# Performance work log

Measured on AMD Instinct MI355X. Metric: run time of the kernel, lower is better.

Reference implementation:

```python
import jax, jax.numpy as jnp
import numpy as np

B, T, IN, H, OUT = 64, 256, 512, 1024, 512

def setup_inputs() -> dict:
    key = jax.random.key(0)
    k1, k2, k3, k4 = jax.random.split(key, 4)
    xs = jax.random.normal(k1, (B, T, IN), dtype=jnp.float32)
    # fused gate projections (order: i, f, g, o), scaled like lecun_normal-ish init
    Wi = jax.random.normal(k2, (IN, 4 * H), dtype=jnp.float32) * (1.0 / np.sqrt(IN))
    Wh = jax.random.normal(k3, (H, 4 * H), dtype=jnp.float32) * (1.0 / np.sqrt(H))
    b = jnp.zeros((4 * H,), dtype=jnp.float32)
    Wo = jax.random.normal(k4, (H, OUT), dtype=jnp.float32) * (1.0 / np.sqrt(H))
    bo = jnp.zeros((OUT,), dtype=jnp.float32)
    return {"xs": xs, "Wi": Wi, "Wh": Wh, "b": b, "Wo": Wo, "bo": bo}

def _lstm_scan(xs, Wi, Wh, b):
    # Precompute the input projection for all timesteps at once: [B, T, 4H]
    xp = jnp.einsum('bti,ih->bth', xs, Wi)
    xp = jnp.transpose(xp, (1, 0, 2))  # [T, B, 4H] for scan over time
    h0 = jnp.zeros((xs.shape[0], Wh.shape[0]), dtype=xs.dtype)
    c0 = jnp.zeros_like(h0)
    Hdim = Wh.shape[0]

    def step(carry, xp_t):
        c, h = carry
        gates = xp_t + h @ Wh + b  # [B, 4H]
        i, f, g, o = jnp.split(gates, 4, axis=-1)  # flax order: i, f, g, o
        c_new = jax.nn.sigmoid(f) * c + jax.nn.sigmoid(i) * jnp.tanh(g)
        h_new = jax.nn.sigmoid(o) * jnp.tanh(c_new)
        return (c_new, h_new), h_new

    (_, _), hs = jax.lax.scan(step, (c0, h0), xp)
    return jnp.transpose(hs, (1, 0, 2))  # [B, T, H]

def reference(xs, Wi, Wh, b, Wo, bo):
    zs = _lstm_scan(xs, Wi, Wh, b)          # [B, T, H]
    logits = jnp.einsum('bth,ho->bto', zs, Wo) + bo  # [B, T, OUT]
    return logits
```

## Files before the change

### kernel.cpp

```cpp
#include <hip/hip_runtime.h>
#include <hip/hip_cooperative_groups.h>


#define B_   64
#define T_   256
#define IN_  512
#define H_   1024
#define G4_  4096
#define OUT_ 512
#define KTOT 1536

typedef __bf16 bf8v  __attribute__((ext_vector_type(8)));
typedef float  f4v   __attribute__((ext_vector_type(4)));

__device__ __forceinline__ float sigm(float x) { return 1.f / (1.f + __expf(-x)); }
__device__ __forceinline__ float tanh_f(float x) { return 1.f - 2.f / (__expf(2.f * x) + 1.f); }

__device__ __forceinline__ void store_bf16_wt(__bf16* p, __bf16 v) {
    union { __bf16 b; unsigned short s; } cv; cv.b = v;
    unsigned w = cv.s;
    asm volatile("global_store_short %0, %1, off sc0 sc1"
                 :: "v"(p), "v"(w) : "memory");
}

__device__ __forceinline__ void grid_barrier(unsigned* flags, int t, int blk) {
    __syncthreads();
    const unsigned tgt = (unsigned)(t + 1);
    if (threadIdx.x < 64) {
        if (threadIdx.x == 0) {
            unsigned* p = &flags[blk * 16];
            asm volatile("global_store_dword %0, %1, off sc0 sc1"
                         :: "v"(p), "v"(tgt) : "memory");
        }
        const int lane = threadIdx.x;
        for (;;) {
            unsigned m0 = __hip_atomic_load(&flags[(lane * 4 + 0) * 16],
                                            __ATOMIC_RELAXED, __HIP_MEMORY_SCOPE_AGENT);
            unsigned m1 = __hip_atomic_load(&flags[(lane * 4 + 1) * 16],
                                            __ATOMIC_RELAXED, __HIP_MEMORY_SCOPE_AGENT);
            unsigned m2 = __hip_atomic_load(&flags[(lane * 4 + 2) * 16],
                                            __ATOMIC_RELAXED, __HIP_MEMORY_SCOPE_AGENT);
            unsigned m3 = __hip_atomic_load(&flags[(lane * 4 + 3) * 16],
                                            __ATOMIC_RELAXED, __HIP_MEMORY_SCOPE_AGENT);
            bool ok = (m0 >= tgt) & (m1 >= tgt) & (m2 >= tgt) & (m3 >= tgt);
            if (__all(ok)) break;
            __builtin_amdgcn_s_sleep(1);
        }
        __builtin_amdgcn_fence(__ATOMIC_ACQUIRE, "agent");
    }
    __syncthreads();
}

__global__ void __launch_bounds__(256)
lstm_fused(const float* __restrict__ xs, const float* __restrict__ Wi,
           const float* __restrict__ Wh, const float* __restrict__ bias,
           const float* __restrict__ Wo, const float* __restrict__ bo,
           float* __restrict__ out, __bf16* __restrict__ hws,
           unsigned* __restrict__ flags)
{
    __shared__ __bf16 Wlds[16][KTOT + 8];
    __shared__ float  gbuf[64][17];
    __shared__ float  obuf[4][16][17];

    const int tid = threadIdx.x;
    const int blk = blockIdx.x;
    const int j0  = blk * 4;
    const int ob0 = (blk >> 5) * 8;
    const int oc0 = (blk & 31) * 16;

    for (int idx = tid; idx < 16 * KTOT; idx += 256) {
        int k = idx >> 4, c = idx & 15;
        int gc = (c >> 2) * H_ + j0 + (c & 3);
        float w = (k < IN_) ? Wi[(size_t)k * G4_ + gc]
                            : Wh[(size_t)(k - IN_) * G4_ + gc];
        Wlds[c][k] = (__bf16)w;
    }
    __syncthreads();

    const int lane = tid & 63;
    const int wave = tid >> 6;
    const int c    = lane & 15;
    const int quad = lane >> 4;
    const int rowA = wave * 16 + c;
    const int kq   = quad * 8;

    const float biasv = bias[(c >> 2) * H_ + j0 + (c & 3)];

    bf8v wof[8];
    #pragma unroll
    for (int kk = 0; kk < 8; ++kk) {
        int kbase = wave * 256 + kk * 32 + kq;
        #pragma unroll
        for (int j = 0; j < 8; ++j)
            wof[kk][j] = (__bf16)Wo[(size_t)(kbase + j) * OUT_ + oc0 + c];
    }

    float c_reg = 0.f;
    const int bb = tid >> 2;
    const int jo = tid & 3;

    for (int t = 0; t < T_; ++t) {
        const __bf16* hhi_p = hws + (size_t)(t & 1) * (2 * B_ * H_);
        const __bf16* hlo_p = hhi_p + B_ * H_;
        __bf16* hhi_c = hws + (size_t)((t + 1) & 1) * (2 * B_ * H_);
        __bf16* hlo_c = hhi_c + B_ * H_;

        f4v acc0 = {0.f, 0.f, 0.f, 0.f};
        f4v acc1 = {0.f, 0.f, 0.f, 0.f};
        const float* xrow = xs + ((size_t)rowA * T_ + t) * IN_ + kq;
        #pragma unroll
        for (int ks = 0; ks < 16; ++ks) {
            f4v v0 = *(const f4v*)(xrow + ks * 32);
            f4v v1 = *(const f4v*)(xrow + ks * 32 + 4);
            bf8v ah, al;
            #pragma unroll
            for (int j = 0; j < 4; ++j) {
                __bf16 h0 = (__bf16)v0[j], h1 = (__bf16)v1[j];
                ah[j] = h0;  ah[4 + j] = h1;
                al[j]     = (__bf16)(v0[j] - (float)h0);
                al[4 + j] = (__bf16)(v1[j] - (float)h1);
            }
            bf8v w = *(const bf8v*)&Wlds[c][ks * 32 + kq];
            acc0 = __builtin_amdgcn_mfma_f32_16x16x32_bf16(ah, w, acc0, 0, 0, 0);
            acc1 = __builtin_amdgcn_mfma_f32_16x16x32_bf16(al, w, acc1, 0, 0, 0);
        }
        if (t > 0) {
            const __bf16* hh = hhi_p + (size_t)rowA * H_ + kq;
            const __bf16* hl = hlo_p + (size_t)rowA * H_ + kq;
            #pragma unroll
            for (int ks = 0; ks < 32; ++ks) {
                bf8v ah = *(const bf8v*)(hh + ks * 32);
                bf8v al = *(const bf8v*)(hl + ks * 32);
                bf8v w  = *(const bf8v*)&Wlds[c][IN_ + ks * 32 + kq];
                acc0 = __builtin_amdgcn_mfma_f32_16x16x32_bf16(ah, w, acc0, 0, 0, 0);
                acc1 = __builtin_amdgcn_mfma_f32_16x16x32_bf16(al, w, acc1, 0, 0, 0);
            }
        }
        f4v acc = acc0 + acc1;
        #pragma unroll
        for (int r = 0; r < 4; ++r)
            gbuf[wave * 16 + quad * 4 + r][c] = acc[r] + biasv;

        if (t > 0) {
            f4v oac = {0.f, 0.f, 0.f, 0.f};
            #pragma unroll
            for (int kk = 0; kk < 8; ++kk) {
                int kbase = wave * 256 + kk * 32 + kq;
                bf8v ah = {}, al = {};
                if (c < 8) {
                    ah = *(const bf8v*)&hhi_p[(size_t)(ob0 + c) * H_ + kbase];
                    al = *(const bf8v*)&hlo_p[(size_t)(ob0 + c) * H_ + kbase];
                }
                oac = __builtin_amdgcn_mfma_f32_16x16x32_bf16(ah, wof[kk], oac, 0, 0, 0);
                oac = __builtin_amdgcn_mfma_f32_16x16x32_bf16(al, wof[kk], oac, 0, 0, 0);
            }
            #pragma unroll
            for (int r = 0; r < 4; ++r)
                obuf[wave][quad * 4 + r][c] = oac[r];
        }
        __syncthreads();

        {
            float gi = gbuf[bb][jo];
            float gf = gbuf[bb][4 + jo];
            float gg = gbuf[bb][8 + jo];
            float go = gbuf[bb][12 + jo];
            c_reg = sigm(gf) * c_reg + sigm(gi) * tanh_f(gg);
            float hn = sigm(go) * tanh_f(c_reg);
            __bf16 hh = (__bf16)hn;
            store_bf16_wt(&hhi_c[(size_t)bb * H_ + j0 + jo], hh);
            store_bf16_wt(&hlo_c[(size_t)bb * H_ + j0 + jo], (__bf16)(hn - (float)hh));
        }
        if (t > 0 && tid < 128) {
            int m = tid >> 4, cc = tid & 15;
            float v = obuf[0][m][cc] + obuf[1][m][cc] + obuf[2][m][cc] + obuf[3][m][cc]
                    + bo[oc0 + cc];
            out[(((size_t)(ob0 + m)) * T_ + (t - 1)) * OUT_ + oc0 + cc] = v;
        }

        grid_barrier(flags, t, blk);
    }

    {
        const __bf16* hhi_l = hws;
        const __bf16* hlo_l = hws + B_ * H_;
        f4v oac = {0.f, 0.f, 0.f, 0.f};
        #pragma unroll
        for (int kk = 0; kk < 8; ++kk) {
            int kbase = wave * 256 + kk * 32 + kq;
            bf8v ah = {}, al = {};
            if (c < 8) {
                ah = *(const bf8v*)&hhi_l[(size_t)(ob0 + c) * H_ + kbase];
                al = *(const bf8v*)&hlo_l[(size_t)(ob0 + c) * H_ + kbase];
            }
            oac = __builtin_amdgcn_mfma_f32_16x16x32_bf16(ah, wof[kk], oac, 0, 0, 0);
            oac = __builtin_amdgcn_mfma_f32_16x16x32_bf16(al, wof[kk], oac, 0, 0, 0);
        }
        #pragma unroll
        for (int r = 0; r < 4; ++r)
            obuf[wave][quad * 4 + r][c] = oac[r];
        __syncthreads();
        if (tid < 128) {
            int m = tid >> 4, cc = tid & 15;
            float v = obuf[0][m][cc] + obuf[1][m][cc] + obuf[2][m][cc] + obuf[3][m][cc]
                    + bo[oc0 + cc];
            out[(((size_t)(ob0 + m)) * T_ + (T_ - 1)) * OUT_ + oc0 + cc] = v;
        }
    }
}

extern "C" void kernel_launch(void* const* d_in, const int* in_sizes, int n_in,
                              void* d_out, int out_size, void* d_ws, size_t ws_size,
                              hipStream_t stream) {
    const float* xs = (const float*)d_in[0];
    const float* Wi = (const float*)d_in[1];
    const float* Wh = (const float*)d_in[2];
    const float* b  = (const float*)d_in[3];
    const float* Wo = (const float*)d_in[4];
    const float* bo = (const float*)d_in[5];
    float* out = (float*)d_out;

    unsigned* flags = (unsigned*)d_ws;
    __bf16*   hws   = (__bf16*)((char*)d_ws + 65536);

    hipMemsetAsync(d_ws, 0, 32768, stream);

    void* args[] = {(void*)&xs, (void*)&Wi, (void*)&Wh, (void*)&b,
                    (void*)&Wo, (void*)&bo, (void*)&out, (void*)&hws,
                    (void*)&flags};
    hipLaunchCooperativeKernel((void*)lstm_fused, dim3(256), dim3(256), args, 0, stream);
}
```

Before: 4.237 ms.

## Split gate GEMM K dimension across twice as many waves per block

Doubles the block to 512 threads (8 waves) and splits the reduction dimension of the per-step gate GEMM and the output projection in half across wave groups. Partial sums go to two LDS buffers and are added with the bias in the elementwise step. The aim is to shorten each timestep's serial critical path by giving every wave half the MFMA chain and half the loads. In exchange it adds an extra LDS reduction, only half the threads do the gate nonlinearity, and register or occupancy pressure may rise under the larger launch bound.

```diff
diff --git a/kernel.cpp b/kernel.cpp
--- a/kernel.cpp
+++ b/kernel.cpp
@@ -51,7 +51,7 @@
     __syncthreads();
 }
 
-__global__ void __launch_bounds__(256)
+__global__ void __launch_bounds__(512)
 lstm_fused(const float* __restrict__ xs, const float* __restrict__ Wi,
            const float* __restrict__ Wh, const float* __restrict__ bias,
            const float* __restrict__ Wo, const float* __restrict__ bo,
@@ -59,8 +59,8 @@
            unsigned* __restrict__ flags)
 {
     __shared__ __bf16 Wlds[16][KTOT + 8];
-    __shared__ float  gbuf[64][17];
-    __shared__ float  obuf[4][16][17];
+    __shared__ float  gbufp[2][64][17];
+    __shared__ float  obuf[8][8][17];
 
     const int tid = threadIdx.x;
     const int blk = blockIdx.x;
@@ -68,7 +68,7 @@
     const int ob0 = (blk >> 5) * 8;
     const int oc0 = (blk & 31) * 16;
 
-    for (int idx = tid; idx < 16 * KTOT; idx += 256) {
+    for (int idx = tid; idx < 16 * KTOT; idx += 512) {
         int k = idx >> 4, c = idx & 15;
         int gc = (c >> 2) * H_ + j0 + (c & 3);
         float w = (k < IN_) ? Wi[(size_t)k * G4_ + gc]
@@ -81,15 +81,15 @@
     const int wave = tid >> 6;
     const int c    = lane & 15;
     const int quad = lane >> 4;
-    const int rowA = wave * 16 + c;
+    const int wg   = wave & 3;
+    const int kh   = wave >> 2;
+    const int rowA = wg * 16 + c;
     const int kq   = quad * 8;
 
-    const float biasv = bias[(c >> 2) * H_ + j0 + (c & 3)];
-
-    bf8v wof[8];
+    bf8v wof[4];
     #pragma unroll
-    for (int kk = 0; kk < 8; ++kk) {
-        int kbase = wave * 256 + kk * 32 + kq;
+    for (int kk = 0; kk < 4; ++kk) {
+        int kbase = wave * 128 + kk * 32 + kq;
         #pragma unroll
         for (int j = 0; j < 8; ++j)
             wof[kk][j] = (__bf16)Wo[(size_t)(kbase + j) * OUT_ + oc0 + c];
@@ -98,6 +98,13 @@
     float c_reg = 0.f;
     const int bb = tid >> 2;
     const int jo = tid & 3;
+    float bi0 = 0.f, bi1 = 0.f, bi2 = 0.f, bi3 = 0.f;
+    if (tid < 256) {
+        bi0 = bias[0 * H_ + j0 + jo];
+        bi1 = bias[1 * H_ + j0 + jo];
+        bi2 = bias[2 * H_ + j0 + jo];
+        bi3 = bias[3 * H_ + j0 + jo];
+    }
 
     for (int t = 0; t < T_; ++t) {
         const __bf16* hhi_p = hws + (size_t)(t & 1) * (2 * B_ * H_);
@@ -107,9 +114,9 @@
 
         f4v acc0 = {0.f, 0.f, 0.f, 0.f};
         f4v acc1 = {0.f, 0.f, 0.f, 0.f};
-        const float* xrow = xs + ((size_t)rowA * T_ + t) * IN_ + kq;
-        #pragma unroll
-        for (int ks = 0; ks < 16; ++ks) {
+        const float* xrow = xs + ((size_t)rowA * T_ + t) * IN_ + kh * 256 + kq;
+        #pragma unroll
+        for (int ks = 0; ks < 8; ++ks) {
             f4v v0 = *(const f4v*)(xrow + ks * 32);
             f4v v1 = *(const f4v*)(xrow + ks * 32 + 4);
             bf8v ah, al;
@@ -120,18 +127,18 @@
                 al[j]     = (__bf16)(v0[j] - (float)h0);
                 al[4 + j] = (__bf16)(v1[j] - (float)h1);
             }
-            bf8v w = *(const bf8v*)&Wlds[c][ks * 32 + kq];
+            bf8v w = *(const bf8v*)&Wlds[c][kh * 256 + ks * 32 + kq];
             acc0 = __builtin_amdgcn_mfma_f32_16x16x32_bf16(ah, w, acc0, 0, 0, 0);
             acc1 = __builtin_amdgcn_mfma_f32_16x16x32_bf16(al, w, acc1, 0, 0, 0);
         }
         if (t > 0) {
-            const __bf16* hh = hhi_p + (size_t)rowA * H_ + kq;
-            const __bf16* hl = hlo_p + (size_t)rowA * H_ + kq;
-            #pragma unroll
-            for (int ks = 0; ks < 32; ++ks) {
+            const __bf16* hh = hhi_p + (size_t)rowA * H_ + kh * 512 + kq;
+            const __bf16* hl = hlo_p + (size_t)rowA * H_ + kh * 512 + kq;
+            #pragma unroll
+            for (int ks = 0; ks < 16; ++ks) {
                 bf8v ah = *(const bf8v*)(hh + ks * 32);
                 bf8v al = *(const bf8v*)(hl + ks * 32);
-                bf8v w  = *(const bf8v*)&Wlds[c][IN_ + ks * 32 + kq];
+                bf8v w  = *(const bf8v*)&Wlds[c][IN_ + kh * 512 + ks * 32 + kq];
                 acc0 = __builtin_amdgcn_mfma_f32_16x16x32_bf16(ah, w, acc0, 0, 0, 0);
                 acc1 = __builtin_amdgcn_mfma_f32_16x16x32_bf16(al, w, acc1, 0, 0, 0);
             }
@@ -139,13 +146,13 @@
         f4v acc = acc0 + acc1;
         #pragma unroll
         for (int r = 0; r < 4; ++r)
-            gbuf[wave * 16 + quad * 4 + r][c] = acc[r] + biasv;
+            gbufp[kh][wg * 16 + quad * 4 + r][c] = acc[r];
 
         if (t > 0) {
             f4v oac = {0.f, 0.f, 0.f, 0.f};
             #pragma unroll
-            for (int kk = 0; kk < 8; ++kk) {
-                int kbase = wave * 256 + kk * 32 + kq;
+            for (int kk = 0; kk < 4; ++kk) {
+                int kbase = wave * 128 + kk * 32 + kq;
                 bf8v ah = {}, al = {};
                 if (c < 8) {
                     ah = *(const bf8v*)&hhi_p[(size_t)(ob0 + c) * H_ + kbase];
@@ -154,17 +161,19 @@
                 oac = __builtin_amdgcn_mfma_f32_16x16x32_bf16(ah, wof[kk], oac, 0, 0, 0);
                 oac = __builtin_amdgcn_mfma_f32_16x16x32_bf16(al, wof[kk], oac, 0, 0, 0);
             }
-            #pragma unroll
-            for (int r = 0; r < 4; ++r)
-                obuf[wave][quad * 4 + r][c] = oac[r];
+            if (quad < 2) {
+                #pragma unroll
+                for (int r = 0; r < 4; ++r)
+                    obuf[wave][quad * 4 + r][c] = oac[r];
+            }
         }
         __syncthreads();
 
-        {
-            float gi = gbuf[bb][jo];
-            float gf = gbuf[bb][4 + jo];
-            float gg = gbuf[bb][8 + jo];
-            float go = gbuf[bb][12 + jo];
+        if (tid < 256) {
+            float gi = gbufp[0][bb][jo]      + gbufp[1][bb][jo]      + bi0;
+            float gf = gbufp[0][bb][4 + jo]  + gbufp[1][bb][4 + jo]  + bi1;
+            float gg = gbufp[0][bb][8 + jo]  + gbufp[1][bb][8 + jo]  + bi2;
+            float go = gbufp[0][bb][12 + jo] + gbufp[1][bb][12 + jo] + bi3;
             c_reg = sigm(gf) * c_reg + sigm(gi) * tanh_f(gg);
             float hn = sigm(go) * tanh_f(c_reg);
             __bf16 hh = (__bf16)hn;
@@ -174,6 +183,7 @@
         if (t > 0 && tid < 128) {
             int m = tid >> 4, cc = tid & 15;
             float v = obuf[0][m][cc] + obuf[1][m][cc] + obuf[2][m][cc] + obuf[3][m][cc]
+                    + obuf[4][m][cc] + obuf[5][m][cc] + obuf[6][m][cc] + obuf[7][m][cc]
                     + bo[oc0 + cc];
             out[(((size_t)(ob0 + m)) * T_ + (t - 1)) * OUT_ + oc0 + cc] = v;
         }
@@ -186,8 +196,8 @@
         const __bf16* hlo_l = hws + B_ * H_;
         f4v oac = {0.f, 0.f, 0.f, 0.f};
         #pragma unroll
-        for (int kk = 0; kk < 8; ++kk) {
-            int kbase = wave * 256 + kk * 32 + kq;
+        for (int kk = 0; kk < 4; ++kk) {
+            int kbase = wave * 128 + kk * 32 + kq;
             bf8v ah = {}, al = {};
             if (c < 8) {
                 ah = *(const bf8v*)&hhi_l[(size_t)(ob0 + c) * H_ + kbase];
@@ -196,13 +206,16 @@
             oac = __builtin_amdgcn_mfma_f32_16x16x32_bf16(ah, wof[kk], oac, 0, 0, 0);
             oac = __builtin_amdgcn_mfma_f32_16x16x32_bf16(al, wof[kk], oac, 0, 0, 0);
         }
-        #pragma unroll
-        for (int r = 0; r < 4; ++r)
-            obuf[wave][quad * 4 + r][c] = oac[r];
+        if (quad < 2) {
+            #pragma unroll
+            for (int r = 0; r < 4; ++r)
+                obuf[wave][quad * 4 + r][c] = oac[r];
+        }
         __syncthreads();
         if (tid < 128) {
             int m = tid >> 4, cc = tid & 15;
             float v = obuf[0][m][cc] + obuf[1][m][cc] + obuf[2][m][cc] + obuf[3][m][cc]
+                    + obuf[4][m][cc] + obuf[5][m][cc] + obuf[6][m][cc] + obuf[7][m][cc]
                     + bo[oc0 + cc];
             out[(((size_t)(ob0 + m)) * T_ + (T_ - 1)) * OUT_ + oc0 + cc] = v;
         }
@@ -228,5 +241,5 @@
     void* args[] = {(void*)&xs, (void*)&Wi, (void*)&Wh, (void*)&b,
                     (void*)&Wo, (void*)&bo, (void*)&out, (void*)&hws,
                     (void*)&flags};
-    hipLaunchCooperativeKernel((void*)lstm_fused, dim3(256), dim3(256), args, 0, stream);
-}
+    hipLaunchCooperativeKernel((void*)lstm_fused, dim3(256), dim3(512), args, 0, stream);
+}
```

After: 4.553 ms. 7.4% more time.

## Overlap next-step input projection with grid barrier wait

Applied to the files above, without the earlier changes.

Splits the grid barrier into arrive and wait phases. Between them, each block computes the input-projection MFMAs (x_{t+1} times Wi, with the bf16 hi/lo split) for the next timestep. This hides that work inside barrier latency and takes it off the serial recurrence critical path. In exchange it keeps two extra accumulators live across the loop, and launch_bounds now pins one block per SM.

```diff
diff --git a/kernel.cpp b/kernel.cpp
--- a/kernel.cpp
+++ b/kernel.cpp
@@ -23,35 +23,28 @@
                  :: "v"(p), "v"(w) : "memory");
 }
 
-__device__ __forceinline__ void grid_barrier(unsigned* flags, int t, int blk) {
-    __syncthreads();
-    const unsigned tgt = (unsigned)(t + 1);
-    if (threadIdx.x < 64) {
-        if (threadIdx.x == 0) {
-            unsigned* p = &flags[blk * 16];
-            asm volatile("global_store_dword %0, %1, off sc0 sc1"
-                         :: "v"(p), "v"(tgt) : "memory");
-        }
-        const int lane = threadIdx.x;
-        for (;;) {
-            unsigned m0 = __hip_atomic_load(&flags[(lane * 4 + 0) * 16],
-                                            __ATOMIC_RELAXED, __HIP_MEMORY_SCOPE_AGENT);
-            unsigned m1 = __hip_atomic_load(&flags[(lane * 4 + 1) * 16],
-                                            __ATOMIC_RELAXED, __HIP_MEMORY_SCOPE_AGENT);
-            unsigned m2 = __hip_atomic_load(&flags[(lane * 4 + 2) * 16],
-                                            __ATOMIC_RELAXED, __HIP_MEMORY_SCOPE_AGENT);
-            unsigned m3 = __hip_atomic_load(&flags[(lane * 4 + 3) * 16],
-                                            __ATOMIC_RELAXED, __HIP_MEMORY_SCOPE_AGENT);
-            bool ok = (m0 >= tgt) & (m1 >= tgt) & (m2 >= tgt) & (m3 >= tgt);
-            if (__all(ok)) break;
-            __builtin_amdgcn_s_sleep(1);
-        }
-        __builtin_amdgcn_fence(__ATOMIC_ACQUIRE, "agent");
-    }
-    __syncthreads();
-}
-
-__global__ void __launch_bounds__(256)
+#define X_PRE(tt, xa0, xa1)                                                   \
+    {                                                                         \
+        const float* xrow = xs + ((size_t)rowA * T_ + (size_t)(tt)) * IN_ + kq; \
+        _Pragma("unroll")                                                     \
+        for (int ks = 0; ks < 16; ++ks) {                                     \
+            f4v v0 = *(const f4v*)(xrow + ks * 32);                           \
+            f4v v1 = *(const f4v*)(xrow + ks * 32 + 4);                       \
+            bf8v ah, al;                                                      \
+            _Pragma("unroll")                                                 \
+            for (int j = 0; j < 4; ++j) {                                     \
+                __bf16 h0 = (__bf16)v0[j], h1 = (__bf16)v1[j];                \
+                ah[j] = h0;  ah[4 + j] = h1;                                  \
+                al[j]     = (__bf16)(v0[j] - (float)h0);                      \
+                al[4 + j] = (__bf16)(v1[j] - (float)h1);                      \
+            }                                                                 \
+            bf8v w = *(const bf8v*)&Wlds[c][ks * 32 + kq];                    \
+            xa0 = __builtin_amdgcn_mfma_f32_16x16x32_bf16(ah, w, xa0, 0, 0, 0); \
+            xa1 = __builtin_amdgcn_mfma_f32_16x16x32_bf16(al, w, xa1, 0, 0, 0); \
+        }                                                                     \
+    }
+
+__global__ void __launch_bounds__(256, 1)
 lstm_fused(const float* __restrict__ xs, const float* __restrict__ Wi,
            const float* __restrict__ Wh, const float* __restrict__ bias,
            const float* __restrict__ Wo, const float* __restrict__ bo,
@@ -99,31 +92,18 @@
     const int bb = tid >> 2;
     const int jo = tid & 3;
 
+    f4v xacc0 = {0.f, 0.f, 0.f, 0.f};
+    f4v xacc1 = {0.f, 0.f, 0.f, 0.f};
+    X_PRE(0, xacc0, xacc1);
+
     for (int t = 0; t < T_; ++t) {
         const __bf16* hhi_p = hws + (size_t)(t & 1) * (2 * B_ * H_);
         const __bf16* hlo_p = hhi_p + B_ * H_;
         __bf16* hhi_c = hws + (size_t)((t + 1) & 1) * (2 * B_ * H_);
         __bf16* hlo_c = hhi_c + B_ * H_;
 
-        f4v acc0 = {0.f, 0.f, 0.f, 0.f};
-        f4v acc1 = {0.f, 0.f, 0.f, 0.f};
-        const float* xrow = xs + ((size_t)rowA * T_ + t) * IN_ + kq;
-        #pragma unroll
-        for (int ks = 0; ks < 16; ++ks) {
-            f4v v0 = *(const f4v*)(xrow + ks * 32);
-            f4v v1 = *(const f4v*)(xrow + ks * 32 + 4);
-            bf8v ah, al;
-            #pragma unroll
-            for (int j = 0; j < 4; ++j) {
-                __bf16 h0 = (__bf16)v0[j], h1 = (__bf16)v1[j];
-                ah[j] = h0;  ah[4 + j] = h1;
-                al[j]     = (__bf16)(v0[j] - (float)h0);
-                al[4 + j] = (__bf16)(v1[j] - (float)h1);
-            }
-            bf8v w = *(const bf8v*)&Wlds[c][ks * 32 + kq];
-            acc0 = __builtin_amdgcn_mfma_f32_16x16x32_bf16(ah, w, acc0, 0, 0, 0);
-            acc1 = __builtin_amdgcn_mfma_f32_16x16x32_bf16(al, w, acc1, 0, 0, 0);
-        }
+        f4v acc0 = xacc0;
+        f4v acc1 = xacc1;
         if (t > 0) {
             const __bf16* hh = hhi_p + (size_t)rowA * H_ + kq;
             const __bf16* hl = hlo_p + (size_t)rowA * H_ + kq;
@@ -178,7 +158,37 @@
             out[(((size_t)(ob0 + m)) * T_ + (t - 1)) * OUT_ + oc0 + cc] = v;
         }
 
-        grid_barrier(flags, t, blk);
+        __syncthreads();
+        const unsigned tgt = (unsigned)(t + 1);
+        if (tid == 0) {
+            unsigned* p = &flags[blk * 16];
+            asm volatile("global_store_dword %0, %1, off sc0 sc1"
+                         :: "v"(p), "v"(tgt) : "memory");
+        }
+        xacc0 = (f4v){0.f, 0.f, 0.f, 0.f};
+        xacc1 = (f4v){0.f, 0.f, 0.f, 0.f};
+        if (t + 1 < T_) {
+            X_PRE(t + 1, xacc0, xacc1);
+        }
+        asm volatile("" ::: "memory");
+        if (tid < 64) {
+            const int lane2 = tid;
+            for (;;) {
+                unsigned m0 = __hip_atomic_load(&flags[(lane2 * 4 + 0) * 16],
+                                                __ATOMIC_RELAXED, __HIP_MEMORY_SCOPE_AGENT);
+                unsigned m1 = __hip_atomic_load(&flags[(lane2 * 4 + 1) * 16],
+                                                __ATOMIC_RELAXED, __HIP_MEMORY_SCOPE_AGENT);
+                unsigned m2 = __hip_atomic_load(&flags[(lane2 * 4 + 2) * 16],
+                                                __ATOMIC_RELAXED, __HIP_MEMORY_SCOPE_AGENT);
+                unsigned m3 = __hip_atomic_load(&flags[(lane2 * 4 + 3) * 16],
+                                                __ATOMIC_RELAXED, __HIP_MEMORY_SCOPE_AGENT);
+                bool ok = (m0 >= tgt) & (m1 >= tgt) & (m2 >= tgt) & (m3 >= tgt);
+                if (__all(ok)) break;
+                __builtin_amdgcn_s_sleep(1);
+            }
+            __builtin_amdgcn_fence(__ATOMIC_ACQUIRE, "agent");
+        }
+        __syncthreads();
     }
 
     {
```

Measured after the change: 4.133 ms. 2.5% less time.
